# Optimization experiments

Measured on AMD Instinct MI355X. Metric: run time of the kernel, lower is better.

Reference implementation:

```python
import jax, jax.numpy as jnp
from jax import lax
import numpy as np

EPS = 1e-5

def _conv_bn(x, w, g, b, m, v):
    # 3x3 VALID conv (no bias) + inference BatchNorm, no relu
    y = lax.conv_general_dilated(x, w, window_strides=(1, 1), padding='VALID',
                                 dimension_numbers=('NCHW', 'OIHW', 'NCHW'))
    inv = g * lax.rsqrt(v + EPS)                      # [C]
    return y * inv[None, :, None, None] + (b - m * inv)[None, :, None, None]

def _xcorr_depthwise(z, x):
    # z: [B,C,hz,wz] kernel, x: [B,C,hx,wx] search -> [B,C,hx-hz+1,wx-wz+1]
    C = z.shape[1]
    def one(zi, xi):
        return lax.conv_general_dilated(xi[None], zi[:, None], (1, 1), 'VALID',
                                        dimension_numbers=('NCHW', 'OIHW', 'NCHW'),
                                        feature_group_count=C)[0]
    return jax.vmap(one)(z, x)

def setup_inputs() -> dict:
    key = jax.random.key(0)
    B, Cin, H = 32, 256, 256
    ks = jax.random.split(key, 30)
    d = {
        'z': jax.random.normal(ks[0], (B, Cin, 8, 8), jnp.float32),
        'x': jax.random.normal(ks[1], (B, Cin, 32, 32), jnp.float32),
    }
    i = 2
    for p in ['cls_z', 'cls_x', 'reg_z', 'reg_x']:
        d[p + '_w'] = 0.01 * jax.random.normal(ks[i], (H, Cin, 3, 3), jnp.float32); i += 1
        d[p + '_g'] = jnp.ones((H,), jnp.float32)
        d[p + '_b'] = jnp.zeros((H,), jnp.float32)
        d[p + '_m'] = 0.1 * jax.random.normal(ks[i], (H,), jnp.float32); i += 1
        d[p + '_v'] = jax.random.uniform(ks[i], (H,), jnp.float32, 0.5, 1.5); i += 1
    return d

def reference(z, x,
              cls_z_w, cls_z_g, cls_z_b, cls_z_m, cls_z_v,
              cls_x_w, cls_x_g, cls_x_b, cls_x_m, cls_x_v,
              reg_z_w, reg_z_g, reg_z_b, reg_z_m, reg_z_v,
              reg_x_w, reg_x_g, reg_x_b, reg_x_m, reg_x_v):
    cls_z = _conv_bn(z, cls_z_w, cls_z_g, cls_z_b, cls_z_m, cls_z_v)
    cls_x = _conv_bn(x, cls_x_w, cls_x_g, cls_x_b, cls_x_m, cls_x_v)
    cls_out = _xcorr_depthwise(cls_z, cls_x)
    reg_z = _conv_bn(z, reg_z_w, reg_z_g, reg_z_b, reg_z_m, reg_z_v)
    reg_x = _conv_bn(x, reg_x_w, reg_x_g, reg_x_b, reg_x_m, reg_x_v)
    reg_out = _xcorr_depthwise(reg_z, reg_x)
    return (cls_out, reg_out)
```

## Files before the change

kernel.cpp:

```cpp
#include <hip/hip_runtime.h>

#define EPS 1e-5f

typedef __attribute__((ext_vector_type(8))) short bf16x8;
typedef __attribute__((ext_vector_type(4))) float f32x4;
typedef __attribute__((ext_vector_type(4))) unsigned short u16x4;
typedef unsigned short ushort_t;

__device__ __forceinline__ ushort_t f2bf(float f) {
  unsigned u = __float_as_uint(f);
  unsigned r = (u + 0x7fffu + ((u >> 16) & 1u)) >> 16;
  return (ushort_t)r;
}
__device__ __forceinline__ float bf2f(ushort_t h) {
  return __uint_as_float((unsigned)h << 16);
}

#define GLDS16(g, l) __builtin_amdgcn_global_load_lds( \
    (const __attribute__((address_space(1))) void*)(g), \
    (__attribute__((address_space(3))) void*)(l), 16, 0, 0)

__global__ __launch_bounds__(256) void pack_kernel(
    const float* __restrict__ x, const float* __restrict__ z,
    const float* __restrict__ wxa, const float* __restrict__ wxb,
    const float* __restrict__ wza, const float* __restrict__ wzb,
    ushort_t* __restrict__ xh, ushort_t* __restrict__ zh,
    ushort_t* __restrict__ Bxo, ushort_t* __restrict__ Bzo)
{
  __shared__ ushort_t t[64 * 260];
  int id = blockIdx.x;
  int tid = threadIdx.x;
  if (id < 1024) {
    int b = id >> 5, h = id & 31;
    const float* src = x + (size_t)b * 262144 + h * 32;
#pragma unroll
    for (int it = 0; it < 8; ++it) {
      int f = it * 256 + tid;
      int c = f >> 3, wq = f & 7;
      float4 v = *reinterpret_cast<const float4*>(src + c * 1024 + wq * 4);
      t[(4 * wq + 0) * 260 + c] = f2bf(v.x);
      t[(4 * wq + 1) * 260 + c] = f2bf(v.y);
      t[(4 * wq + 2) * 260 + c] = f2bf(v.z);
      t[(4 * wq + 3) * 260 + c] = f2bf(v.w);
    }
    __syncthreads();
    ushort_t* dst = xh + (size_t)(b * 32 + h) * 8192;
#pragma unroll
    for (int it = 0; it < 8; ++it) {
      int Q = it * 256 + tid;
      int w = Q >> 6, c0 = (Q & 63) * 4;
      u16x4 pk = *reinterpret_cast<const u16x4*>(&t[w * 260 + c0]);
      *reinterpret_cast<u16x4*>(&dst[w * 256 + c0]) = pk;
    }
  } else if (id < 1056) {
    int b = id - 1024;
    const float* src = z + (size_t)b * 16384;
#pragma unroll
    for (int it = 0; it < 16; ++it) {
      int f = it * 256 + tid;
      int c = f >> 4, hq = f & 15;
      float4 v = *reinterpret_cast<const float4*>(src + c * 64 + hq * 4);
      t[(4 * hq + 0) * 260 + c] = f2bf(v.x);
      t[(4 * hq + 1) * 260 + c] = f2bf(v.y);
      t[(4 * hq + 2) * 260 + c] = f2bf(v.z);
      t[(4 * hq + 3) * 260 + c] = f2bf(v.w);
    }
    __syncthreads();
    ushort_t* dst = zh + (size_t)b * 16384;
#pragma unroll
    for (int it = 0; it < 16; ++it) {
      int Q = it * 256 + tid;
      int hw = Q >> 6, c0 = (Q & 63) * 4;
      u16x4 pk = *reinterpret_cast<const u16x4*>(&t[hw * 260 + c0]);
      *reinterpret_cast<u16x4*>(&dst[hw * 256 + c0]) = pk;
    }
  } else {
    float* tf = reinterpret_cast<float*>(t);
    int wid = id - 1056;
    int isZ = wid >> 9;
    int n   = wid & 511;
    const float* s0 = isZ ? wza : wxa;
    const float* s1 = isZ ? wzb : wxb;
    const float* src = (n < 256 ? s0 : s1) + (size_t)(n & 255) * 2304;
#pragma unroll
    for (int it = 0; it < 3; ++it) {
      int f = it * 256 + tid;
      if (f < 576) {
        float4 v = *reinterpret_cast<const float4*>(src + f * 4);
        *reinterpret_cast<float4*>(&tf[f * 4]) = v;
      }
    }
    __syncthreads();
    ushort_t* dst = (isZ ? Bzo : Bxo) + (size_t)n * 2304;
#pragma unroll
    for (int it = 0; it < 9; ++it) {
      int k = it * 256 + tid;
      int tap = k >> 8, ci = k & 255;
      dst[k] = f2bf(tf[ci * 9 + tap]);
    }
  }
}

template<int OW, int OWH, int IW, int IMG, typename OutT>
__device__ __forceinline__ void conv_body(
    int mtile, int ntile,
    const ushort_t* __restrict__ Aimg, const ushort_t* __restrict__ Bw,
    const float* __restrict__ g0, const float* __restrict__ b0,
    const float* __restrict__ m0, const float* __restrict__ v0,
    const float* __restrict__ g1, const float* __restrict__ b1,
    const float* __restrict__ m1, const float* __restrict__ v1,
    OutT* __restrict__ out0, OutT* __restrict__ out1,
    ushort_t* As, ushort_t* Bs)
{
  const int tid  = threadIdx.x;
  const int lane = tid & 63;
  const int wave = tid >> 6;
  const int wr   = wave >> 1, wc = wave & 1;

  const int chunk = (tid & 7) ^ ((tid >> 3) & 7);
  int abase[4], bbase[4];
#pragma unroll
  for (int i = 0; i < 4; ++i) {
    int row = i * 32 + (tid >> 3);
    int m_g = mtile * 128 + row;
    int b   = m_g / OWH;
    int s   = m_g - b * OWH;
    int oh  = s / OW;
    int ow  = s - oh * OW;
    abase[i] = (b * IMG + oh * IW + ow) * 256 + chunk * 8;
    int n_g = ntile * 128 + row;
    bbase[i] = n_g * 2304 + chunk * 8;
  }

  f32x4 acc[4][4];
#pragma unroll
  for (int i = 0; i < 4; ++i)
#pragma unroll
    for (int j = 0; j < 4; ++j)
      acc[i][j] = (f32x4){0.f, 0.f, 0.f, 0.f};

  const int lrow = lane & 15;
  const int lk   = lane >> 4;
  const int rA   = wr * 64;
  const int rB   = wc * 64;
  const int sw   = lrow & 7;

  for (int ks = 0; ks < 36; ++ks) {
    const int k0  = ks * 64;
    const int tap = k0 >> 8;
    const int ci0 = k0 & 255;
    const int kh  = tap / 3;
    const int kw  = tap - kh * 3;
    const int aoff = (kh * IW + kw) * 256 + ci0;
#pragma unroll
    for (int i = 0; i < 4; ++i) {
      GLDS16(Aimg + abase[i] + aoff, &As[(i * 256 + tid) * 8]);
      GLDS16(Bw + bbase[i] + k0,     &Bs[(i * 256 + tid) * 8]);
    }
    __syncthreads();
#pragma unroll
    for (int kc = 0; kc < 2; ++kc) {
      bf16x8 af[4], bfr[4];
#pragma unroll
      for (int mi = 0; mi < 4; ++mi)
        af[mi] = *(const bf16x8*)&As[(rA + mi * 16 + lrow) * 64 + (((kc << 2) | lk) ^ sw) * 8];
#pragma unroll
      for (int ni = 0; ni < 4; ++ni)
        bfr[ni] = *(const bf16x8*)&Bs[(rB + ni * 16 + lrow) * 64 + (((kc << 2) | lk) ^ sw) * 8];
#pragma unroll
      for (int mi = 0; mi < 4; ++mi)
#pragma unroll
        for (int ni = 0; ni < 4; ++ni)
          acc[mi][ni] = __builtin_amdgcn_mfma_f32_16x16x32_bf16(
              af[mi], bfr[ni], acc[mi][ni], 0, 0, 0);
    }
    __syncthreads();
  }

#pragma unroll
  for (int ni = 0; ni < 4; ++ni) {
    int n_g  = ntile * 128 + rB + ni * 16 + lrow;
    int path = n_g >> 8;
    int co   = n_g & 255;
    const float* G  = path ? g1 : g0;
    const float* Bb = path ? b1 : b0;
    const float* Mm = path ? m1 : m0;
    const float* Vv = path ? v1 : v0;
    float iv = G[co] * rsqrtf(Vv[co] + EPS);
    float be = Bb[co] - Mm[co] * iv;
    OutT* outp = path ? out1 : out0;
#pragma unroll
    for (int mi = 0; mi < 4; ++mi) {
      int m_g = mtile * 128 + rA + mi * 16 + lk * 4;
      int b   = m_g / OWH;
      int s   = m_g - b * OWH;
      if constexpr (sizeof(OutT) == 2) {
        u16x4 pk;
#pragma unroll
        for (int r = 0; r < 4; ++r) pk[r] = f2bf(acc[mi][ni][r] * iv + be);
        *reinterpret_cast<u16x4*>(&outp[(size_t)(b * 256 + co) * OWH + s]) = pk;
      } else {
        f32x4 pk;
#pragma unroll
        for (int r = 0; r < 4; ++r) pk[r] = acc[mi][ni][r] * iv + be;
        *reinterpret_cast<f32x4*>(&outp[(size_t)(b * 256 + co) * OWH + s]) = pk;
      }
    }
  }
}

__global__ __launch_bounds__(256) void conv_fused_kernel(
    const ushort_t* __restrict__ xh, const ushort_t* __restrict__ zh,
    const ushort_t* __restrict__ Bx, const ushort_t* __restrict__ Bz,
    const float* Gcx, const float* Bcx, const float* Mcx, const float* Vcx,
    const float* Grx, const float* Brx, const float* Mrx, const float* Vrx,
    const float* Gcz, const float* Bcz, const float* Mcz, const float* Vcz,
    const float* Grz, const float* Brz, const float* Mrz, const float* Vrz,
    ushort_t* __restrict__ cls_xf, ushort_t* __restrict__ reg_xf,
    float* __restrict__ cls_zf, float* __restrict__ reg_zf)
{
  __shared__ ushort_t As[128 * 64];
  __shared__ ushort_t Bs[128 * 64];
  int bid = blockIdx.x;
  if (bid < 900) {
    int xcd = bid & 7, within = bid >> 3;
    int id = (xcd < 4 ? xcd * 113 : 452 + (xcd - 4) * 112) + within;
    conv_body<30, 900, 32, 1024, ushort_t>(id >> 2, id & 3, xh, Bx,
        Gcx, Bcx, Mcx, Vcx, Grx, Brx, Mrx, Vrx, cls_xf, reg_xf, As, Bs);
  } else {
    int j = bid - 900;
    conv_body<6, 36, 8, 64, float>(j >> 2, j & 3, zh, Bz,
        Gcz, Bcz, Mcz, Vcz, Grz, Brz, Mrz, Vrz, cls_zf, reg_zf, As, Bs);
  }
}

__global__ __launch_bounds__(256) void xcorr_kernel(
    const float* __restrict__ cls_zf, const float* __restrict__ reg_zf,
    const ushort_t* __restrict__ cls_xf, const ushort_t* __restrict__ reg_xf,
    float* __restrict__ out)
{
  int id   = blockIdx.x;
  int path = id >> 13;
  int bc   = id & 8191;
  int tid  = threadIdx.x;
  __shared__ float szs[36];
  __shared__ float sx[900];
  const float*    zp = (path ? reg_zf : cls_zf) + (size_t)bc * 36;
  const ushort_t* xp = (path ? reg_xf : cls_xf) + (size_t)bc * 900;
  if (tid < 225) {
    u16x4 v = *reinterpret_cast<const u16x4*>(xp + tid * 4);
    sx[tid * 4 + 0] = bf2f(v[0]);
    sx[tid * 4 + 1] = bf2f(v[1]);
    sx[tid * 4 + 2] = bf2f(v[2]);
    sx[tid * 4 + 3] = bf2f(v[3]);
  }
  if (tid < 36) szs[tid] = zp[tid];
  __syncthreads();
  float zreg[36];
#pragma unroll
  for (int i = 0; i < 36; ++i) zreg[i] = szs[i];
  float* op = out + (size_t)path * 5120000 + (size_t)bc * 625;
  for (int pos = tid; pos < 625; pos += 256) {
    int p = pos / 25, q = pos % 25;
    float acc = 0.f;
#pragma unroll
    for (int u = 0; u < 6; ++u)
#pragma unroll
      for (int v = 0; v < 6; ++v)
        acc += zreg[u * 6 + v] * sx[(p + u) * 30 + (q + v)];
    op[pos] = acc;
  }
}

extern "C" void kernel_launch(void* const* d_in, const int* in_sizes, int n_in,
                              void* d_out, int out_size, void* d_ws, size_t ws_size,
                              hipStream_t stream) {
  const float* z = (const float*)d_in[0];
  const float* x = (const float*)d_in[1];
  const float *W[4], *G[4], *Bb[4], *M[4], *V[4];
  for (int p = 0; p < 4; ++p) {
    W[p]  = (const float*)d_in[2 + p * 5 + 0];
    G[p]  = (const float*)d_in[2 + p * 5 + 1];
    Bb[p] = (const float*)d_in[2 + p * 5 + 2];
    M[p]  = (const float*)d_in[2 + p * 5 + 3];
    V[p]  = (const float*)d_in[2 + p * 5 + 4];
  }

  char* ws = (char*)d_ws;
  ushort_t* xhwc   = (ushort_t*)ws; ws += (size_t)32*32*32*256 * 2;
  ushort_t* zhwc   = (ushort_t*)ws; ws += (size_t)32*8*8*256 * 2;
  ushort_t* Bx     = (ushort_t*)ws; ws += (size_t)512*2304 * 2;
  ushort_t* Bz     = (ushort_t*)ws; ws += (size_t)512*2304 * 2;
  ushort_t* cls_xf = (ushort_t*)ws; ws += (size_t)32*256*900 * 2;
  ushort_t* reg_xf = (ushort_t*)ws; ws += (size_t)32*256*900 * 2;
  float* cls_zf    = (float*)ws;    ws += (size_t)32*256*36 * 4;
  float* reg_zf    = (float*)ws;

  float* outF = (float*)d_out;

  pack_kernel<<<2080, 256, 0, stream>>>(x, z, W[1], W[3], W[0], W[2],
                                        xhwc, zhwc, Bx, Bz);
  conv_fused_kernel<<<936, 256, 0, stream>>>(
      xhwc, zhwc, Bx, Bz,
      G[1], Bb[1], M[1], V[1], G[3], Bb[3], M[3], V[3],
      G[0], Bb[0], M[0], V[0], G[2], Bb[2], M[2], V[2],
      cls_xf, reg_xf, cls_zf, reg_zf);
  xcorr_kernel<<<16384, 256, 0, stream>>>(cls_zf, reg_zf, cls_xf, reg_xf, outF);
}
```

Measured before the change: 268.0 us.

## Double-buffer conv LDS staging and register-block the xcorr kernel

The implicit-GEMM conv now uses two LDS buffers, so global_load_lds for the next K-step is issued before the MFMA work on the current step, hiding load latency behind compute. The xcorr kernel now handles two channels per block and computes five adjacent outputs per thread from a register window of ten inputs per row, which cuts LDS reads and index arithmetic. The trade-offs are that LDS per conv block doubles to 64KB, which can limit occupancy, and xcorr output stores become strided per thread.

```diff
diff --git a/kernel.cpp b/kernel.cpp
--- a/kernel.cpp
+++ b/kernel.cpp
@@ -110,7 +110,7 @@
     const float* __restrict__ g1, const float* __restrict__ b1,
     const float* __restrict__ m1, const float* __restrict__ v1,
     OutT* __restrict__ out0, OutT* __restrict__ out1,
-    ushort_t* As, ushort_t* Bs)
+    ushort_t* lds)
 {
   const int tid  = threadIdx.x;
   const int lane = tid & 63;
@@ -132,32 +132,43 @@
     bbase[i] = n_g * 2304 + chunk * 8;
   }
 
-  f32x4 acc[4][4];
-#pragma unroll
-  for (int i = 0; i < 4; ++i)
-#pragma unroll
-    for (int j = 0; j < 4; ++j)
-      acc[i][j] = (f32x4){0.f, 0.f, 0.f, 0.f};
-
-  const int lrow = lane & 15;
-  const int lk   = lane >> 4;
-  const int rA   = wr * 64;
-  const int rB   = wc * 64;
-  const int sw   = lrow & 7;
-
-  for (int ks = 0; ks < 36; ++ks) {
+  auto stage = [&](int buf, int ks) {
     const int k0  = ks * 64;
     const int tap = k0 >> 8;
     const int ci0 = k0 & 255;
     const int kh  = tap / 3;
     const int kw  = tap - kh * 3;
     const int aoff = (kh * IW + kw) * 256 + ci0;
+    ushort_t* dstA = lds + buf * 16384;
+    ushort_t* dstB = dstA + 8192;
 #pragma unroll
     for (int i = 0; i < 4; ++i) {
-      GLDS16(Aimg + abase[i] + aoff, &As[(i * 256 + tid) * 8]);
-      GLDS16(Bw + bbase[i] + k0,     &Bs[(i * 256 + tid) * 8]);
-    }
-    __syncthreads();
+      GLDS16(Aimg + abase[i] + aoff, &dstA[(i * 256 + tid) * 8]);
+      GLDS16(Bw + bbase[i] + k0,     &dstB[(i * 256 + tid) * 8]);
+    }
+  };
+
+  f32x4 acc[4][4];
+#pragma unroll
+  for (int i = 0; i < 4; ++i)
+#pragma unroll
+    for (int j = 0; j < 4; ++j)
+      acc[i][j] = (f32x4){0.f, 0.f, 0.f, 0.f};
+
+  const int lrow = lane & 15;
+  const int lk   = lane >> 4;
+  const int rA   = wr * 64;
+  const int rB   = wc * 64;
+  const int sw   = lrow & 7;
+
+  stage(0, 0);
+  __syncthreads();
+
+  for (int ks = 0; ks < 36; ++ks) {
+    const int cur = ks & 1;
+    if (ks < 35) stage(cur ^ 1, ks + 1);
+    const ushort_t* As = lds + cur * 16384;
+    const ushort_t* Bs = As + 8192;
 #pragma unroll
     for (int kc = 0; kc < 2; ++kc) {
       bf16x8 af[4], bfr[4];
@@ -219,18 +230,17 @@
     ushort_t* __restrict__ cls_xf, ushort_t* __restrict__ reg_xf,
     float* __restrict__ cls_zf, float* __restrict__ reg_zf)
 {
-  __shared__ ushort_t As[128 * 64];
-  __shared__ ushort_t Bs[128 * 64];
+  __shared__ ushort_t lds[2 * 16384];
   int bid = blockIdx.x;
   if (bid < 900) {
     int xcd = bid & 7, within = bid >> 3;
     int id = (xcd < 4 ? xcd * 113 : 452 + (xcd - 4) * 112) + within;
     conv_body<30, 900, 32, 1024, ushort_t>(id >> 2, id & 3, xh, Bx,
-        Gcx, Bcx, Mcx, Vcx, Grx, Brx, Mrx, Vrx, cls_xf, reg_xf, As, Bs);
+        Gcx, Bcx, Mcx, Vcx, Grx, Brx, Mrx, Vrx, cls_xf, reg_xf, lds);
   } else {
     int j = bid - 900;
     conv_body<6, 36, 8, 64, float>(j >> 2, j & 3, zh, Bz,
-        Gcz, Bcz, Mcz, Vcz, Grz, Brz, Mrz, Vrz, cls_zf, reg_zf, As, Bs);
+        Gcz, Bcz, Mcz, Vcz, Grz, Brz, Mrz, Vrz, cls_zf, reg_zf, lds);
   }
 }
 
@@ -239,36 +249,55 @@
     const ushort_t* __restrict__ cls_xf, const ushort_t* __restrict__ reg_xf,
     float* __restrict__ out)
 {
-  int id   = blockIdx.x;
-  int path = id >> 13;
-  int bc   = id & 8191;
-  int tid  = threadIdx.x;
-  __shared__ float szs[36];
-  __shared__ float sx[900];
+  int bid   = blockIdx.x;
+  int path  = bid >> 12;
+  int pair0 = (bid & 4095) * 2;
+  int tid   = threadIdx.x;
+  int half  = tid >> 7;
+  int t     = tid & 127;
+  int bc    = pair0 + half;
+  __shared__ float sx[2][912];
   const float*    zp = (path ? reg_zf : cls_zf) + (size_t)bc * 36;
   const ushort_t* xp = (path ? reg_xf : cls_xf) + (size_t)bc * 900;
-  if (tid < 225) {
-    u16x4 v = *reinterpret_cast<const u16x4*>(xp + tid * 4);
-    sx[tid * 4 + 0] = bf2f(v[0]);
-    sx[tid * 4 + 1] = bf2f(v[1]);
-    sx[tid * 4 + 2] = bf2f(v[2]);
-    sx[tid * 4 + 3] = bf2f(v[3]);
-  }
-  if (tid < 36) szs[tid] = zp[tid];
+  {
+    u16x4 v = *reinterpret_cast<const u16x4*>(xp + t * 4);
+    sx[half][t * 4 + 0] = bf2f(v[0]);
+    sx[half][t * 4 + 1] = bf2f(v[1]);
+    sx[half][t * 4 + 2] = bf2f(v[2]);
+    sx[half][t * 4 + 3] = bf2f(v[3]);
+    if (t < 97) {
+      u16x4 w = *reinterpret_cast<const u16x4*>(xp + (t + 128) * 4);
+      sx[half][(t + 128) * 4 + 0] = bf2f(w[0]);
+      sx[half][(t + 128) * 4 + 1] = bf2f(w[1]);
+      sx[half][(t + 128) * 4 + 2] = bf2f(w[2]);
+      sx[half][(t + 128) * 4 + 3] = bf2f(w[3]);
+    }
+  }
+  float zreg[36];
+#pragma unroll
+  for (int i = 0; i < 36; ++i) zreg[i] = zp[i];
   __syncthreads();
-  float zreg[36];
-#pragma unroll
-  for (int i = 0; i < 36; ++i) zreg[i] = szs[i];
-  float* op = out + (size_t)path * 5120000 + (size_t)bc * 625;
-  for (int pos = tid; pos < 625; pos += 256) {
-    int p = pos / 25, q = pos % 25;
-    float acc = 0.f;
-#pragma unroll
-    for (int u = 0; u < 6; ++u)
-#pragma unroll
-      for (int v = 0; v < 6; ++v)
-        acc += zreg[u * 6 + v] * sx[(p + u) * 30 + (q + v)];
-    op[pos] = acc;
+  if (t < 125) {
+    int p = t / 5, q0 = (t % 5) * 5;
+    float a0 = 0.f, a1 = 0.f, a2 = 0.f, a3 = 0.f, a4 = 0.f;
+#pragma unroll
+    for (int u = 0; u < 6; ++u) {
+      const float* row = &sx[half][(p + u) * 30 + q0];
+      float xw[10];
+#pragma unroll
+      for (int w = 0; w < 10; ++w) xw[w] = row[w];
+#pragma unroll
+      for (int v = 0; v < 6; ++v) {
+        float zv = zreg[u * 6 + v];
+        a0 += zv * xw[v];
+        a1 += zv * xw[v + 1];
+        a2 += zv * xw[v + 2];
+        a3 += zv * xw[v + 3];
+        a4 += zv * xw[v + 4];
+      }
+    }
+    float* op = out + (size_t)path * 5120000 + (size_t)bc * 625 + p * 25 + q0;
+    op[0] = a0; op[1] = a1; op[2] = a2; op[3] = a3; op[4] = a4;
   }
 }
 
@@ -305,5 +334,5 @@
       G[1], Bb[1], M[1], V[1], G[3], Bb[3], M[3], V[3],
       G[0], Bb[0], M[0], V[0], G[2], Bb[2], M[2], V[2],
       cls_xf, reg_xf, cls_zf, reg_zf);
-  xcorr_kernel<<<16384, 256, 0, stream>>>(cls_zf, reg_zf, cls_xf, reg_xf, outF);
-}
+  xcorr_kernel<<<8192, 256, 0, stream>>>(cls_zf, reg_zf, cls_xf, reg_xf, outF);
+}
```

Result: faster. 240.1 us (-10.4%).
